# Performance work log

Hardware: AMD Instinct MI355X
Metric: run time of the kernel (lower is better)

## Reference

```python
import jax, jax.numpy as jnp
import numpy as np


def setup_inputs() -> dict:
    key = jax.random.key(0)
    k1, k2, k3, k4 = jax.random.split(key, 4)
    B, S, D = 2, 2048, 1024
    return {
        "X": jax.random.normal(k1, (B, S, D), dtype=jnp.float32),
        "W_q": jax.random.normal(k2, (D, D), dtype=jnp.float32),
        "W_k": jax.random.normal(k3, (D, D), dtype=jnp.float32),
        "W_v": jax.random.normal(k4, (D, D), dtype=jnp.float32),
        "n_heads": 16,
    }


def reference(X, W_q, W_k, W_v, n_heads):
    B, S, D = X.shape
    H = n_heads
    dh = D // H
    # QKV projections, split heads: [B,S,D] -> [H,B,S,dh]
    def split_heads(Y):
        return Y.reshape(B, S, H, dh).transpose(2, 0, 1, 3)
    Q = split_heads(X @ W_q)
    K = split_heads(X @ W_k)
    V = split_heads(X @ W_v)
    scale = 1.0 / jnp.sqrt(jnp.asarray(dh, dtype=X.dtype))
    # [H,B,S,S] attention scores (naive, matches the original)
    scores = jax.nn.softmax(jnp.einsum("hbqd,hbkd->hbqk", Q, K) * scale, axis=-1)
    out = jnp.einsum("hbqk,hbkd->hbqd", scores, V)  # [H,B,S,dh]
    # torch.concat(out, 0) over leading H dim -> [H*B, S, dh]
    return out.reshape(H * B, S, dh)
```

## Files before the change

### kernel.cpp

```cpp
#include <hip/hip_runtime.h>

typedef unsigned short u16;
typedef unsigned int u32;
typedef __bf16 bf16x8 __attribute__((ext_vector_type(8)));
typedef float f32x4 __attribute__((ext_vector_type(4)));
typedef float f32x16 __attribute__((ext_vector_type(16)));

extern "C" __device__ float __ocml_native_exp2_f32(float);

#define WT_HI_E  ((size_t)0)
#define WT_LO_E  ((size_t)3 << 20)
#define X_HI_E   ((size_t)6 << 20)
#define X_LO_E   ((size_t)10 << 20)
#define Q_HI_E   ((size_t)14 << 20)
#define Q_LO_E   ((size_t)18 << 20)
#define K_HI_E   ((size_t)22 << 20)
#define K_LO_E   ((size_t)26 << 20)
#define V_HI_E   ((size_t)30 << 20)

__device__ __forceinline__ u16 bf16_rne(float x) {
  u32 u = __float_as_uint(x);
  u32 r = (u + 0x7fffu + ((u >> 16) & 1u)) >> 16;
  return (u16)r;
}
__device__ __forceinline__ float bf16_f(u16 h) {
  return __uint_as_float(((u32)h) << 16);
}

__device__ __forceinline__ void gload16(const u16* g, u16* l) {
  __builtin_amdgcn_global_load_lds(
      (const __attribute__((address_space(1))) void*)g,
      (__attribute__((address_space(3))) void*)l, 16, 0, 0);
}

__global__ __launch_bounds__(256) void k_split(const float* __restrict__ X,
                                               const float* __restrict__ w0,
                                               const float* __restrict__ w1,
                                               const float* __restrict__ w2,
                                               u16* __restrict__ ws) {
  int bid = blockIdx.x;
  if (bid < 2048) {
    u16* xh = ws + X_HI_E;
    u16* xl = ws + X_LO_E;
    size_t i = ((size_t)bid * 256 + threadIdx.x) * 8;
    float4 a = *(const float4*)(X + i);
    float4 b = *(const float4*)(X + i + 4);
    float v[8] = {a.x, a.y, a.z, a.w, b.x, b.y, b.z, b.w};
    u32 Hh[4], Ll[4];
#pragma unroll
    for (int j = 0; j < 4; j++) {
      u16 h0 = bf16_rne(v[2 * j]);
      u16 l0 = bf16_rne(v[2 * j] - bf16_f(h0));
      u16 h1 = bf16_rne(v[2 * j + 1]);
      u16 l1 = bf16_rne(v[2 * j + 1] - bf16_f(h1));
      Hh[j] = (u32)h0 | ((u32)h1 << 16);
      Ll[j] = (u32)l0 | ((u32)l1 << 16);
    }
    *(uint4*)(xh + i) = make_uint4(Hh[0], Hh[1], Hh[2], Hh[3]);
    *(uint4*)(xl + i) = make_uint4(Ll[0], Ll[1], Ll[2], Ll[3]);
  } else {
    int wb = bid - 2048;
    int z = wb >> 10;
    int rem = wb & 1023;
    int by = (rem >> 5) * 32, bx = (rem & 31) * 32;
    const float* W = (z == 0) ? w0 : ((z == 1) ? w1 : w2);
    u16* th = ws + WT_HI_E + (size_t)z * (1u << 20);
    u16* tl = ws + WT_LO_E + (size_t)z * (1u << 20);
    __shared__ float tile[32][33];
    int tx = threadIdx.x & 31, ty = threadIdx.x >> 5;
#pragma unroll
    for (int i = 0; i < 4; i++) {
      int r = ty + i * 8;
      tile[r][tx] = W[(size_t)(by + r) * 1024 + bx + tx];
    }
    __syncthreads();
#pragma unroll
    for (int i = 0; i < 4; i++) {
      int r = ty + i * 8;
      float v = tile[tx][r];
      int n = bx + r, k = by + tx;
      u16 h = bf16_rne(v);
      u16 l = bf16_rne(v - bf16_f(h));
      th[(size_t)n * 1024 + k] = h;
      tl[(size_t)n * 1024 + k] = l;
    }
  }
}

__global__ __launch_bounds__(256, 4) void k_proj(u16* __restrict__ ws) {
  int id = blockIdx.x;
  int xcd = id & 7;
  int loc = id >> 3;
  int m_loc = loc & 7;
  int rest = loc >> 3;
  int n_blk = rest & 7, z = rest >> 3;
  int M0 = (xcd * 8 + m_loc) * 64;
  int N0 = n_blk * 128;

  const u16* Xh = ws + X_HI_E;
  const u16* Xl = ws + X_LO_E;
  const u16* Wh = ws + WT_HI_E + (size_t)z * (1u << 20);
  const u16* Wl = ws + WT_LO_E + (size_t)z * (1u << 20);
  u16* dsth = ws + ((z == 0) ? Q_HI_E : ((z == 1) ? K_HI_E : V_HI_E));
  u16* dstl = (z == 0) ? (ws + Q_LO_E) : ((z == 1) ? (ws + K_LO_E) : (u16*)0);

  __shared__ u16 sXh[2048], sXl[2048], sWh[4096], sWl[4096];
  int tid = threadIdx.x, lane = tid & 63, w = tid >> 6;
  int quad = lane >> 4, l16 = lane & 15;
  int mb = (w & 1) * 32, nb = (w >> 1) * 64;

  const f32x4 z4 = {0.f, 0.f, 0.f, 0.f};
  f32x4 acc[2][4];
#pragma unroll
  for (int i = 0; i < 2; i++)
#pragma unroll
    for (int j = 0; j < 4; j++) acc[i][j] = z4;

  int xrow = tid >> 2, xq8 = tid & 3;

  for (int kk = 0; kk < 1024; kk += 32) {
    __syncthreads();
    {
      size_t gx = (size_t)(M0 + xrow) * 1024 + kk + xq8 * 8;
      gload16(Xh + gx, &sXh[(size_t)(w * 16) * 32]);
      if (z != 2) gload16(Xl + gx, &sXl[(size_t)(w * 16) * 32]);
#pragma unroll
      for (int j = 0; j < 2; j++) {
        int c = tid + 256 * j;
        int row = c >> 2, q8 = c & 3;
        size_t gw = (size_t)(N0 + row) * 1024 + kk + q8 * 8;
        gload16(Wh + gw, &sWh[(size_t)(j * 64 + w * 16) * 32]);
        if (z != 2) gload16(Wl + gw, &sWl[(size_t)(j * 64 + w * 16) * 32]);
      }
    }
    __syncthreads();
    bf16x8 ah[2], bh[4];
#pragma unroll
    for (int i = 0; i < 2; i++)
      ah[i] = *(const bf16x8*)&sXh[(mb + i * 16 + l16) * 32 + quad * 8];
#pragma unroll
    for (int j = 0; j < 4; j++)
      bh[j] = *(const bf16x8*)&sWh[(nb + j * 16 + l16) * 32 + quad * 8];
    if (z != 2) {
      bf16x8 al[2], bl[4];
#pragma unroll
      for (int i = 0; i < 2; i++)
        al[i] = *(const bf16x8*)&sXl[(mb + i * 16 + l16) * 32 + quad * 8];
#pragma unroll
      for (int j = 0; j < 4; j++)
        bl[j] = *(const bf16x8*)&sWl[(nb + j * 16 + l16) * 32 + quad * 8];
#pragma unroll
      for (int i = 0; i < 2; i++)
#pragma unroll
        for (int j = 0; j < 4; j++) {
          f32x4 c0 = acc[i][j];
          c0 = __builtin_amdgcn_mfma_f32_16x16x32_bf16(ah[i], bh[j], c0, 0, 0, 0);
          c0 = __builtin_amdgcn_mfma_f32_16x16x32_bf16(ah[i], bl[j], c0, 0, 0, 0);
          c0 = __builtin_amdgcn_mfma_f32_16x16x32_bf16(al[i], bh[j], c0, 0, 0, 0);
          acc[i][j] = c0;
        }
    } else {
#pragma unroll
      for (int i = 0; i < 2; i++)
#pragma unroll
        for (int j = 0; j < 4; j++)
          acc[i][j] = __builtin_amdgcn_mfma_f32_16x16x32_bf16(ah[i], bh[j], acc[i][j], 0, 0, 0);
    }
  }

  if (z == 2) {
#pragma unroll
    for (int i = 0; i < 2; i++)
#pragma unroll
      for (int j = 0; j < 4; j++) {
        int mg = M0 + mb + i * 16 + quad * 4;
        int ng = N0 + nb + j * 16 + l16;
        int b = mg >> 11, s = mg & 2047;
        int hh = ng >> 6, d = ng & 63;
        int cp = ((s >> 3) & 7) ^ (d & 7);
        int ssw = (s & ~63) | (cp << 3) | (s & 7);
        u16 p0 = bf16_rne(acc[i][j][0]);
        u16 p1 = bf16_rne(acc[i][j][1]);
        u16 p2 = bf16_rne(acc[i][j][2]);
        u16 p3 = bf16_rne(acc[i][j][3]);
        *(uint2*)&dsth[((size_t)(hh * 2 + b) * 64 + d) * 2048 + ssw] =
            make_uint2((u32)p0 | ((u32)p1 << 16), (u32)p2 | ((u32)p3 << 16));
      }
  } else {
    float qscale = (z == 0) ? (0.125f * 1.4426950408889634f) : 1.0f;
#pragma unroll
    for (int i = 0; i < 2; i++)
#pragma unroll
      for (int j = 0; j < 4; j++)
#pragma unroll
        for (int r = 0; r < 4; r++) {
          int mg = M0 + mb + i * 16 + quad * 4 + r;
          int ng = N0 + nb + j * 16 + l16;
          int b = mg >> 11, s = mg & 2047;
          int hh = ng >> 6, d = ng & 63;
          int d2 = d;
          if (z == 1) d2 = ((((d >> 3) ^ (s & 7)) & 7) << 3) | (d & 7);
          size_t idx = ((size_t)(hh * 2 + b) * 2048 + s) * 64 + d2;
          float y = acc[i][j][r] * qscale;
          u16 h = bf16_rne(y);
          dsth[idx] = h;
          dstl[idx] = bf16_rne(y - bf16_f(h));
        }
  }
}

__global__ __launch_bounds__(256, 2) void k_attn(u16* __restrict__ ws,
                                                 float* __restrict__ out) {
  const u16* Qh = ws + Q_HI_E;
  const u16* Ql = ws + Q_LO_E;
  const u16* Kh = ws + K_HI_E;
  const u16* Kl = ws + K_LO_E;
  const u16* Vt = ws + V_HI_E;

  __shared__ u16 sKh[2][64][64], sKl[2][64][64], sVt[2][64][64];

  int id = blockIdx.x;
  int hb = id & 31, qb = id >> 5;
  int tid = threadIdx.x, w = tid >> 6, lane = tid & 63;
  int l31 = lane & 31, h = lane >> 5;
  size_t base = (size_t)hb * (2048 * 64);
  int qw0 = qb * 128 + w * 32;

  int srow = lane >> 3, sch = lane & 7;

  auto stage = [&](int buf, int kt) {
#pragma unroll
    for (int b2 = 0; b2 < 2; b2++) {
      int rr = w * 16 + b2 * 8;
      size_t kg = base + (size_t)(kt + rr + srow) * 64 + sch * 8;
      gload16(Kh + kg, &sKh[buf][rr][0]);
      gload16(Kl + kg, &sKl[buf][rr][0]);
      size_t vg = base + (size_t)(rr + srow) * 2048 + kt + sch * 8;
      gload16(Vt + vg, &sVt[buf][rr][0]);
    }
  };

  stage(0, 0);

  bf16x8 qh[4], ql[4];
#pragma unroll
  for (int ks = 0; ks < 4; ks++) {
    size_t off = base + (size_t)(qw0 + l31) * 64 + ks * 16 + h * 8;
    qh[ks] = *(const bf16x8*)(Qh + off);
    ql[ks] = *(const bf16x8*)(Ql + off);
  }

  f32x16 o[2];
#pragma unroll
  for (int i = 0; i < 16; i++) { o[0][i] = 0.f; o[1][i] = 0.f; }
  float mr = -1e30f, lr = 0.f;

  auto rdA = [&](const u16 t[64][64], int mt, int ks) -> bf16x8 {
    int ch = ((ks * 2 + h) ^ (l31 & 7)) * 8;
    return *(const bf16x8*)&t[mt * 32 + l31][ch];
  };

  for (int it = 0; it < 32; it++) {
    __syncthreads();
    if (it + 1 < 32) stage((it + 1) & 1, (it + 1) * 64);
    int buf = it & 1;

    f32x16 sc[2];
#pragma unroll
    for (int i = 0; i < 16; i++) { sc[0][i] = 0.f; sc[1][i] = 0.f; }
#pragma unroll
    for (int ks = 0; ks < 4; ks++)
#pragma unroll
      for (int mt = 0; mt < 2; mt++) {
        bf16x8 kh = rdA(sKh[buf], mt, ks);
        bf16x8 kl = rdA(sKl[buf], mt, ks);
        sc[mt] = __builtin_amdgcn_mfma_f32_32x32x16_bf16(kh, qh[ks], sc[mt], 0, 0, 0);
        sc[mt] = __builtin_amdgcn_mfma_f32_32x32x16_bf16(kh, ql[ks], sc[mt], 0, 0, 0);
        sc[mt] = __builtin_amdgcn_mfma_f32_32x32x16_bf16(kl, qh[ks], sc[mt], 0, 0, 0);
      }

    float mx = sc[0][0];
#pragma unroll
    for (int i = 0; i < 16; i++) {
      mx = fmaxf(mx, sc[0][i]);
      mx = fmaxf(mx, sc[1][i]);
    }
    mx = fmaxf(mx, __shfl_xor(mx, 32));
    float mnew = fmaxf(mr, mx);
    float alpha = __ocml_native_exp2_f32(mr - mnew);
    mr = mnew;
    float rs = 0.f;
    u32 pk[2][8];
#pragma unroll
    for (int t = 0; t < 2; t++)
#pragma unroll
      for (int i = 0; i < 8; i++) {
        float p0 = __ocml_native_exp2_f32(sc[t][2 * i] - mnew);
        float p1 = __ocml_native_exp2_f32(sc[t][2 * i + 1] - mnew);
        rs += p0 + p1;
        u32 a = __float_as_uint(p0) + 0x8000u;
        u32 b = __float_as_uint(p1) + 0x8000u;
        pk[t][i] = __builtin_amdgcn_perm(b, a, 0x07060302u);
      }
    rs += __shfl_xor(rs, 32);
    lr = lr * alpha + rs;
#pragma unroll
    for (int i = 0; i < 16; i++) {
      o[0][i] *= alpha;
      o[1][i] *= alpha;
    }

#pragma unroll
    for (int ks = 0; ks < 4; ks++) {
      int t = ks >> 1, c = ks & 1;
      u32 b0 = pk[t][c * 4 + 0], b1 = pk[t][c * 4 + 1];
      u32 b2 = pk[t][c * 4 + 2], b3 = pk[t][c * 4 + 3];
      u32 rA = (u32)__shfl_xor((int)(h ? b0 : b2), 32);
      u32 rB = (u32)__shfl_xor((int)(h ? b1 : b3), 32);
      uint4 fb = h ? make_uint4(rA, rB, b2, b3) : make_uint4(b0, b1, rA, rB);
      bf16x8 pfrag = *(bf16x8*)&fb;
#pragma unroll
      for (int mt = 0; mt < 2; mt++) {
        bf16x8 vb = rdA(sVt[buf], mt, ks);
        o[mt] = __builtin_amdgcn_mfma_f32_32x32x16_bf16(vb, pfrag, o[mt], 0, 0, 0);
      }
    }
  }

  float inv = 1.f / lr;
  size_t grow = (size_t)hb * 2048 + qw0 + l31;
#pragma unroll
  for (int mt = 0; mt < 2; mt++)
#pragma unroll
    for (int g2 = 0; g2 < 4; g2++) {
      int d0 = mt * 32 + g2 * 8 + 4 * h;
      float4 v = make_float4(o[mt][g2 * 4 + 0] * inv, o[mt][g2 * 4 + 1] * inv,
                             o[mt][g2 * 4 + 2] * inv, o[mt][g2 * 4 + 3] * inv);
      *(float4*)(out + grow * 64 + d0) = v;
    }
}

extern "C" void kernel_launch(void* const* d_in, const int* in_sizes, int n_in,
                              void* d_out, int out_size, void* d_ws, size_t ws_size,
                              hipStream_t stream) {
  const float* X = (const float*)d_in[0];
  const float* Wq = (const float*)d_in[1];
  const float* Wk = (const float*)d_in[2];
  const float* Wv = (const float*)d_in[3];
  u16* ws = (u16*)d_ws;
  float* out = (float*)d_out;

  k_split<<<dim3(5120), dim3(256), 0, stream>>>(X, Wq, Wk, Wv, ws);
  k_proj<<<dim3(1536), dim3(256), 0, stream>>>(ws);
  k_attn<<<dim3(512), dim3(256), 0, stream>>>(ws, out);
}
```

Before: 236.1 us.

## Enlarge projection GEMM tile, vectorize weight transpose-split and Q/K stores

```diff
diff --git a/kernel.cpp b/kernel.cpp
--- a/kernel.cpp
+++ b/kernel.cpp
@@ -60,41 +60,55 @@
     *(uint4*)(xl + i) = make_uint4(Ll[0], Ll[1], Ll[2], Ll[3]);
   } else {
     int wb = bid - 2048;
-    int z = wb >> 10;
-    int rem = wb & 1023;
-    int by = (rem >> 5) * 32, bx = (rem & 31) * 32;
+    int z = wb >> 8;
+    int rem = wb & 255;
+    int by = (rem >> 4) * 64, bx = (rem & 15) * 64;
     const float* W = (z == 0) ? w0 : ((z == 1) ? w1 : w2);
     u16* th = ws + WT_HI_E + (size_t)z * (1u << 20);
     u16* tl = ws + WT_LO_E + (size_t)z * (1u << 20);
-    __shared__ float tile[32][33];
-    int tx = threadIdx.x & 31, ty = threadIdx.x >> 5;
+    __shared__ float tile[64][65];
+    int tx = threadIdx.x & 15, ty = threadIdx.x >> 4;
 #pragma unroll
     for (int i = 0; i < 4; i++) {
-      int r = ty + i * 8;
-      tile[r][tx] = W[(size_t)(by + r) * 1024 + bx + tx];
+      int r = ty + i * 16;
+      float4 v = *(const float4*)(W + (size_t)(by + r) * 1024 + bx + tx * 4);
+      tile[r][tx * 4 + 0] = v.x;
+      tile[r][tx * 4 + 1] = v.y;
+      tile[r][tx * 4 + 2] = v.z;
+      tile[r][tx * 4 + 3] = v.w;
     }
     __syncthreads();
 #pragma unroll
-    for (int i = 0; i < 4; i++) {
-      int r = ty + i * 8;
-      float v = tile[tx][r];
-      int n = bx + r, k = by + tx;
-      u16 h = bf16_rne(v);
-      u16 l = bf16_rne(v - bf16_f(h));
-      th[(size_t)n * 1024 + k] = h;
-      tl[(size_t)n * 1024 + k] = l;
-    }
-  }
-}
-
-__global__ __launch_bounds__(256, 4) void k_proj(u16* __restrict__ ws) {
+    for (int p = 0; p < 2; p++) {
+      int t = threadIdx.x + 256 * p;
+      int kc = t & 7, nl = t >> 3;
+      u32 Hh[4], Ll[4];
+#pragma unroll
+      for (int u = 0; u < 4; u++) {
+        float v0 = tile[kc * 8 + 2 * u][nl];
+        float v1 = tile[kc * 8 + 2 * u + 1][nl];
+        u16 h0 = bf16_rne(v0);
+        u16 l0 = bf16_rne(v0 - bf16_f(h0));
+        u16 h1 = bf16_rne(v1);
+        u16 l1 = bf16_rne(v1 - bf16_f(h1));
+        Hh[u] = (u32)h0 | ((u32)h1 << 16);
+        Ll[u] = (u32)l0 | ((u32)l1 << 16);
+      }
+      size_t o = (size_t)(bx + nl) * 1024 + by + kc * 8;
+      *(uint4*)(th + o) = make_uint4(Hh[0], Hh[1], Hh[2], Hh[3]);
+      *(uint4*)(tl + o) = make_uint4(Ll[0], Ll[1], Ll[2], Ll[3]);
+    }
+  }
+}
+
+__global__ __launch_bounds__(256, 3) void k_proj(u16* __restrict__ ws) {
   int id = blockIdx.x;
   int xcd = id & 7;
   int loc = id >> 3;
-  int m_loc = loc & 7;
-  int rest = loc >> 3;
+  int m_loc = loc & 3;
+  int rest = loc >> 2;
   int n_blk = rest & 7, z = rest >> 3;
-  int M0 = (xcd * 8 + m_loc) * 64;
+  int M0 = (xcd * 4 + m_loc) * 128;
   int N0 = n_blk * 128;
 
   const u16* Xh = ws + X_HI_E;
@@ -104,64 +118,62 @@
   u16* dsth = ws + ((z == 0) ? Q_HI_E : ((z == 1) ? K_HI_E : V_HI_E));
   u16* dstl = (z == 0) ? (ws + Q_LO_E) : ((z == 1) ? (ws + K_LO_E) : (u16*)0);
 
-  __shared__ u16 sXh[2048], sXl[2048], sWh[4096], sWl[4096];
+  __shared__ u16 sXh[4096], sXl[4096], sWh[4096], sWl[4096];
   int tid = threadIdx.x, lane = tid & 63, w = tid >> 6;
   int quad = lane >> 4, l16 = lane & 15;
-  int mb = (w & 1) * 32, nb = (w >> 1) * 64;
+  int mb = (w & 1) * 64, nb = (w >> 1) * 64;
 
   const f32x4 z4 = {0.f, 0.f, 0.f, 0.f};
-  f32x4 acc[2][4];
-#pragma unroll
-  for (int i = 0; i < 2; i++)
+  f32x4 acc[4][4];
+#pragma unroll
+  for (int i = 0; i < 4; i++)
 #pragma unroll
     for (int j = 0; j < 4; j++) acc[i][j] = z4;
-
-  int xrow = tid >> 2, xq8 = tid & 3;
 
   for (int kk = 0; kk < 1024; kk += 32) {
     __syncthreads();
-    {
-      size_t gx = (size_t)(M0 + xrow) * 1024 + kk + xq8 * 8;
-      gload16(Xh + gx, &sXh[(size_t)(w * 16) * 32]);
-      if (z != 2) gload16(Xl + gx, &sXl[(size_t)(w * 16) * 32]);
-#pragma unroll
-      for (int j = 0; j < 2; j++) {
-        int c = tid + 256 * j;
-        int row = c >> 2, q8 = c & 3;
-        size_t gw = (size_t)(N0 + row) * 1024 + kk + q8 * 8;
-        gload16(Wh + gw, &sWh[(size_t)(j * 64 + w * 16) * 32]);
-        if (z != 2) gload16(Wl + gw, &sWl[(size_t)(j * 64 + w * 16) * 32]);
+#pragma unroll
+    for (int j = 0; j < 2; j++) {
+      int c = tid + 256 * j;
+      int row = c >> 2, q8 = c & 3;
+      size_t gx = (size_t)(M0 + row) * 1024 + kk + q8 * 8;
+      size_t gw = (size_t)(N0 + row) * 1024 + kk + q8 * 8;
+      gload16(Xh + gx, &sXh[(size_t)(j * 64 + w * 16) * 32]);
+      gload16(Wh + gw, &sWh[(size_t)(j * 64 + w * 16) * 32]);
+      if (z != 2) {
+        gload16(Xl + gx, &sXl[(size_t)(j * 64 + w * 16) * 32]);
+        gload16(Wl + gw, &sWl[(size_t)(j * 64 + w * 16) * 32]);
       }
     }
     __syncthreads();
-    bf16x8 ah[2], bh[4];
-#pragma unroll
-    for (int i = 0; i < 2; i++)
+    bf16x8 ah[4], bh[4];
+#pragma unroll
+    for (int i = 0; i < 4; i++)
       ah[i] = *(const bf16x8*)&sXh[(mb + i * 16 + l16) * 32 + quad * 8];
 #pragma unroll
     for (int j = 0; j < 4; j++)
       bh[j] = *(const bf16x8*)&sWh[(nb + j * 16 + l16) * 32 + quad * 8];
     if (z != 2) {
-      bf16x8 al[2], bl[4];
-#pragma unroll
-      for (int i = 0; i < 2; i++)
+      bf16x8 al[4], bl[4];
+#pragma unroll
+      for (int i = 0; i < 4; i++)
         al[i] = *(const bf16x8*)&sXl[(mb + i * 16 + l16) * 32 + quad * 8];
 #pragma unroll
       for (int j = 0; j < 4; j++)
         bl[j] = *(const bf16x8*)&sWl[(nb + j * 16 + l16) * 32 + quad * 8];
 #pragma unroll
-      for (int i = 0; i < 2; i++)
-#pragma unroll
-        for (int j = 0; j < 4; j++) {
-          f32x4 c0 = acc[i][j];
-          c0 = __builtin_amdgcn_mfma_f32_16x16x32_bf16(ah[i], bh[j], c0, 0, 0, 0);
-          c0 = __builtin_amdgcn_mfma_f32_16x16x32_bf16(ah[i], bl[j], c0, 0, 0, 0);
-          c0 = __builtin_amdgcn_mfma_f32_16x16x32_bf16(al[i], bh[j], c0, 0, 0, 0);
-          acc[i][j] = c0;
+      for (int j = 0; j < 4; j++)
+#pragma unroll
+        for (int i = 0; i < 4; i++) {
+          f32x4 c0 = acc[j][i];
+          c0 = __builtin_amdgcn_mfma_f32_16x16x32_bf16(bh[j], ah[i], c0, 0, 0, 0);
+          c0 = __builtin_amdgcn_mfma_f32_16x16x32_bf16(bh[j], al[i], c0, 0, 0, 0);
+          c0 = __builtin_amdgcn_mfma_f32_16x16x32_bf16(bl[j], ah[i], c0, 0, 0, 0);
+          acc[j][i] = c0;
         }
     } else {
 #pragma unroll
-      for (int i = 0; i < 2; i++)
+      for (int i = 0; i < 4; i++)
 #pragma unroll
         for (int j = 0; j < 4; j++)
           acc[i][j] = __builtin_amdgcn_mfma_f32_16x16x32_bf16(ah[i], bh[j], acc[i][j], 0, 0, 0);
@@ -170,7 +182,7 @@
 
   if (z == 2) {
 #pragma unroll
-    for (int i = 0; i < 2; i++)
+    for (int i = 0; i < 4; i++)
 #pragma unroll
       for (int j = 0; j < 4; j++) {
         int mg = M0 + mb + i * 16 + quad * 4;
@@ -189,23 +201,28 @@
   } else {
     float qscale = (z == 0) ? (0.125f * 1.4426950408889634f) : 1.0f;
 #pragma unroll
-    for (int i = 0; i < 2; i++)
-#pragma unroll
-      for (int j = 0; j < 4; j++)
+    for (int j = 0; j < 4; j++)
+#pragma unroll
+      for (int i = 0; i < 4; i++) {
+        int ng = N0 + nb + j * 16 + quad * 4;
+        int mg = M0 + mb + i * 16 + l16;
+        int b = mg >> 11, s = mg & 2047;
+        int hh = ng >> 6, d0 = ng & 63;
+        int d2 = d0;
+        if (z == 1) d2 = ((((d0 >> 3) ^ (s & 7)) & 7) << 3) | (d0 & 7);
+        size_t idx = ((size_t)(hh * 2 + b) * 2048 + s) * 64 + d2;
+        u16 h[4], l[4];
 #pragma unroll
         for (int r = 0; r < 4; r++) {
-          int mg = M0 + mb + i * 16 + quad * 4 + r;
-          int ng = N0 + nb + j * 16 + l16;
-          int b = mg >> 11, s = mg & 2047;
-          int hh = ng >> 6, d = ng & 63;
-          int d2 = d;
-          if (z == 1) d2 = ((((d >> 3) ^ (s & 7)) & 7) << 3) | (d & 7);
-          size_t idx = ((size_t)(hh * 2 + b) * 2048 + s) * 64 + d2;
-          float y = acc[i][j][r] * qscale;
-          u16 h = bf16_rne(y);
-          dsth[idx] = h;
-          dstl[idx] = bf16_rne(y - bf16_f(h));
+          float y = acc[j][i][r] * qscale;
+          h[r] = bf16_rne(y);
+          l[r] = bf16_rne(y - bf16_f(h[r]));
         }
+        *(uint2*)&dsth[idx] =
+            make_uint2((u32)h[0] | ((u32)h[1] << 16), (u32)h[2] | ((u32)h[3] << 16));
+        *(uint2*)&dstl[idx] =
+            make_uint2((u32)l[0] | ((u32)l[1] << 16), (u32)l[2] | ((u32)l[3] << 16));
+      }
   }
 }
 
@@ -350,7 +367,7 @@
   u16* ws = (u16*)d_ws;
   float* out = (float*)d_out;
 
-  k_split<<<dim3(5120), dim3(256), 0, stream>>>(X, Wq, Wk, Wv, ws);
-  k_proj<<<dim3(1536), dim3(256), 0, stream>>>(ws);
+  k_split<<<dim3(2816), dim3(256), 0, stream>>>(X, Wq, Wk, Wv, ws);
+  k_proj<<<dim3(768), dim3(256), 0, stream>>>(ws);
   k_attn<<<dim3(512), dim3(256), 0, stream>>>(ws, out);
 }
```

Result: slower. 297.0 us (+25.8%).
